# Optimization experiments

Hardware: AMD Instinct MI355X
Metric: run time of the kernel (lower is better)

The kernel has to match this reference:

```python
import jax, jax.numpy as jnp
import numpy as np
import itertools

B, DIM, RES = 128, 384, 16
NH, KD, D = 8, 32, 128            # heads, key_dim, d = attn_ratio*key_dim
NHKD, DH = NH * KD, NH * D        # 256, 1024
N = RES * RES                     # 256 tokens
SCALE = KD ** -0.5


def _bias_idxs():
    pts = list(itertools.product(range(RES), range(RES)))
    offsets, idxs = {}, []
    for p1 in pts:
        for p2 in pts:
            off = (abs(p1[0] - p2[0]), abs(p1[1] - p2[1]))
            if off not in offsets:
                offsets[off] = len(offsets)
            idxs.append(offsets[off])
    return np.array(idxs, dtype=np.int32).reshape(N, N), len(offsets)


def setup_inputs() -> dict:
    key = jax.random.key(0)
    ks = jax.random.split(key, 16)
    idxs, n_off = _bias_idxs()
    s = 0.02
    return {
        "x": jax.random.normal(ks[0], (B, DIM, RES, RES), jnp.float32),
        "q_w": jax.random.normal(ks[1], (NHKD, DIM), jnp.float32) * s,
        "q_b": jnp.zeros((NHKD,), jnp.float32),
        "k_w": jax.random.normal(ks[2], (NHKD, DIM), jnp.float32) * s,
        "k_b": jnp.zeros((NHKD,), jnp.float32),
        "v_w": jax.random.normal(ks[3], (DH, DIM), jnp.float32) * s,
        "v_b": jnp.zeros((DH,), jnp.float32),
        "vl_w": jax.random.normal(ks[4], (DH, 1, 3, 3), jnp.float32) * s,
        "vl_b": jnp.zeros((DH,), jnp.float32),
        "th1_w": jax.random.normal(ks[5], (NH, NH), jnp.float32) * s,
        "th1_b": jnp.zeros((NH,), jnp.float32),
        "th2_w": jax.random.normal(ks[6], (NH, NH), jnp.float32) * s,
        "th2_b": jnp.zeros((NH,), jnp.float32),
        "proj_w": jax.random.normal(ks[7], (DIM, DH), jnp.float32) * s,
        "proj_b": jnp.zeros((DIM,), jnp.float32),
        "attn_bias": jax.random.normal(ks[8], (NH, n_off), jnp.float32) * s,
        "bias_idxs": jnp.asarray(idxs),
    }


def _conv1x1(x, w, b):  # x: [B,C,H,W], w: [O,C]
    return jnp.einsum('bchw,oc->bohw', x, w) + b[:, None, None]


def reference(x, q_w, q_b, k_w, k_b, v_w, v_b, vl_w, vl_b,
              th1_w, th1_b, th2_w, th2_b, proj_w, proj_b,
              attn_bias, bias_idxs):
    Bx, C, H, W = x.shape
    q = _conv1x1(x, q_w, q_b).reshape(Bx, NH, KD, N).transpose(0, 1, 3, 2)  # bhnk
    k = _conv1x1(x, k_w, k_b).reshape(Bx, NH, KD, N)                        # bhkm
    v4 = _conv1x1(x, v_w, v_b)                                              # [B,DH,H,W]
    v_local = jax.lax.conv_general_dilated(
        v4, vl_w, window_strides=(1, 1), padding='SAME',
        dimension_numbers=('NCHW', 'OIHW', 'NCHW'),
        feature_group_count=DH) + vl_b[:, None, None]
    v = v4.reshape(Bx, NH, D, N).transpose(0, 1, 3, 2)                      # bhnd

    attn = jnp.einsum('bhnk,bhkm->bhnm', q, k) * SCALE + attn_bias[:, bias_idxs]
    attn = jnp.einsum('gh,bhnm->bgnm', th1_w, attn) + th1_b[:, None, None]  # talking head 1
    attn = jax.nn.softmax(attn, axis=-1)
    attn = jnp.einsum('gh,bhnm->bgnm', th2_w, attn) + th2_b[:, None, None]  # talking head 2

    o = jnp.einsum('bhnm,bhmd->bhnd', attn, v)
    out = o.transpose(0, 1, 3, 2).reshape(Bx, DH, H, W) + v_local
    out = jax.nn.relu(out)
    return _conv1x1(out, proj_w, proj_b)
```

## Files before the change

kernel.cpp:

```cpp
#include <hip/hip_runtime.h>
#include <hip/hip_bf16.h>

typedef __hip_bfloat16 bf16;
typedef __bf16 bf16v8 __attribute__((ext_vector_type(8)));
typedef float f32x4 __attribute__((ext_vector_type(4)));

#define BB    128
#define DIM   384
#define NTOK  256
#define NH    8
#define KD    32
#define DHEAD 128
#define DH    1024
#define SCALE 0.17677669529663687f
#define LOG2E 1.4426950408889634f

static __device__ __forceinline__ float sf(float x) {
  return (x == x) ? fminf(fmaxf(x, -1e4f), 1e4f) : 0.f;
}

static __device__ __forceinline__ float rfl(float x) {
  return __int_as_float(__builtin_amdgcn_readfirstlane(__float_as_int(x)));
}

#define GLOAD_LDS16(gsrc, ldst)                                                \
  __builtin_amdgcn_global_load_lds(                                            \
      (const __attribute__((address_space(1))) void*)(gsrc),                   \
      (__attribute__((address_space(3))) void*)(ldst), 16, 0, 0)

__global__ __launch_bounds__(256) void k_convert(const float* __restrict__ qw,
    const float* __restrict__ kw, const float* __restrict__ vw,
    const float* __restrict__ pw, bf16* __restrict__ dst) {
  int i = blockIdx.x * 256 + threadIdx.x;
  float v;
  if (i < 98304)       v = qw[i];
  else if (i < 196608) v = kw[i - 98304];
  else if (i < 589824) v = vw[i - 196608];
  else                 v = pw[i - 589824];
  dst[i] = __float2bfloat16(sf(v));
}

__global__ __launch_bounds__(256) void k_bias(const float* __restrict__ ab,
    const int* __restrict__ idxs, int n_off,
    const float* __restrict__ th1_w, const float* __restrict__ th1_b,
    float* __restrict__ bias_full) {
  int mn = blockIdx.x * 256 + threadIdx.x;
  int m = mn >> 8, n = mn & 255;
  int idx = idxs[n * 256 + m];
  float bh[8];
#pragma unroll
  for (int h = 0; h < 8; ++h) bh[h] = sf(ab[h * n_off + idx]);
#pragma unroll
  for (int g = 0; g < 8; ++g) {
    float a = sf(th1_b[g]);
#pragma unroll
    for (int h = 0; h < 8; ++h) a += sf(th1_w[g * 8 + h]) * bh[h];
    bias_full[((size_t)g * 256 + m) * 256 + n] = a * LOG2E;
  }
}

__global__ __launch_bounds__(256) void k_transpose_x(const float* __restrict__ x,
                                                     bf16* __restrict__ xT) {
  __shared__ bf16 tile[32][33];
  int b = blockIdx.z;
  int c0 = blockIdx.x * 32;
  int n0 = blockIdx.y * 32;
  int t = threadIdx.x;
  int tn = t & 31, tc = t >> 5;
#pragma unroll
  for (int p = 0; p < 4; ++p)
    tile[tc + p * 8][tn] =
        __float2bfloat16(sf(x[((size_t)b * DIM + c0 + tc + p * 8) * NTOK + n0 + tn]));
  __syncthreads();
  int wc = t & 31, wn = t >> 5;
#pragma unroll
  for (int p = 0; p < 4; ++p)
    xT[((size_t)b * NTOK + n0 + wn + p * 8) * DIM + c0 + wc] = tile[wc][wn + p * 8];
}

__global__ __launch_bounds__(256, 3) void k_qkv(const bf16* __restrict__ xT,
    const bf16* __restrict__ W, const float* __restrict__ q_b,
    const float* __restrict__ k_b, const float* __restrict__ v_b,
    bf16* __restrict__ qT, bf16* __restrict__ kT, bf16* __restrict__ v4,
    int nb) {
  __shared__ __align__(16) char smem[34816];
  bf16* sA = (bf16*)smem;
  bf16* sB = (bf16*)(smem + 16384);
  bf16* actt = (bf16*)smem;

  int id = blockIdx.x;
  int b, tile;
  if ((nb & 7) == 0) {
    int per = nb >> 3;
    int xcd = id & 7, slot = id >> 3;
    b = xcd * per + (slot % per);
    tile = slot / per;
  } else { b = id / 24; tile = id % 24; }
  int mt = tile >> 1, nt = tile & 1;
  int m0 = mt * 128, n0b = nt * 128;
  int t = threadIdx.x;
  int wave = t >> 6, lane = t & 63;
  int wm = wave >> 1, wn = wave & 1;
  int qd = lane >> 4, li = lane & 15;
  const bf16* xTb = xT + ((size_t)b * NTOK + n0b) * DIM;

  f32x4 acc[4][4];
#pragma unroll
  for (int r = 0; r < 4; ++r)
#pragma unroll
    for (int f = 0; f < 4; ++f) acc[r][f] = (f32x4){0.f, 0.f, 0.f, 0.f};

  for (int ks = 0; ks < 6; ++ks) {
    int k0 = ks * 64;
    __syncthreads();
#pragma unroll
    for (int i = 0; i < 8; ++i) {
      int g = wave * 512 + i * 64 + lane;
      int gg = g & 1023;
      int row = gg >> 3, slot = gg & 7;
      int col = ((slot ^ (row & 7)) << 3) + k0;
      const bf16* src = (g < 1024)
          ? (W + (size_t)(m0 + row) * DIM + col)
          : (xTb + (size_t)row * DIM + col);
      GLOAD_LDS16(src, smem + (size_t)(wave * 512 + i * 64) * 16);
    }
    __syncthreads();
#pragma unroll
    for (int s = 0; s < 2; ++s) {
      bf16v8 Afr[4], Bfr[4];
#pragma unroll
      for (int r = 0; r < 4; ++r) {
        int row = wm * 64 + r * 16 + li;
        Afr[r] = *(const bf16v8*)(sA + row * 64 + (((s * 4 + qd) ^ (row & 7)) << 3));
      }
#pragma unroll
      for (int f = 0; f < 4; ++f) {
        int row = wn * 64 + f * 16 + li;
        Bfr[f] = *(const bf16v8*)(sB + row * 64 + (((s * 4 + qd) ^ (row & 7)) << 3));
      }
#pragma unroll
      for (int r = 0; r < 4; ++r)
#pragma unroll
        for (int f = 0; f < 4; ++f)
          acc[r][f] = __builtin_amdgcn_mfma_f32_16x16x32_bf16(Afr[r], Bfr[f], acc[r][f], 0, 0, 0);
    }
  }
  __syncthreads();

  if (m0 >= 512) {
    int ch0 = m0 - 512;
#pragma unroll
    for (int r = 0; r < 4; ++r)
#pragma unroll
      for (int f = 0; f < 4; ++f) {
        int coll = wn * 64 + f * 16 + li;
#pragma unroll
        for (int rr = 0; rr < 4; ++rr) {
          int rowl = wm * 64 + r * 16 + qd * 4 + rr;
          actt[rowl * 136 + coll] =
              __float2bfloat16(acc[r][f][rr] + sf(v_b[ch0 + rowl]));
        }
      }
    __syncthreads();
#pragma unroll
    for (int it = 0; it < 8; ++it) {
      int g = it * 256 + t;
      int row = g >> 4, c16 = g & 15;
      bf16v8 vv = *(const bf16v8*)(actt + row * 136 + c16 * 8);
      *(bf16v8*)(v4 + ((size_t)b * DH + ch0 + row) * NTOK + n0b + c16 * 8) = vv;
    }
  } else {
    const float* bias = (m0 < 256) ? q_b : k_b;
    bf16* dst = (m0 < 256) ? qT : kT;
    int mb = (m0 < 256) ? m0 : m0 - 256;
#pragma unroll
    for (int r = 0; r < 4; ++r)
#pragma unroll
      for (int f = 0; f < 4; ++f) {
        int n = n0b + wn * 64 + f * 16 + li;
        int rowg = mb + wm * 64 + r * 16 + qd * 4;
        int h = rowg >> 5, kd = rowg & 31;
        union { bf16 e[4]; uint2 u; } pk;
#pragma unroll
        for (int rr = 0; rr < 4; ++rr)
          pk.e[rr] = __float2bfloat16(acc[r][f][rr] + sf(bias[rowg + rr]));
        *(uint2*)(dst + (((size_t)b * NH + h) * NTOK + n) * KD + kd) = pk.u;
      }
  }
}

__global__ __launch_bounds__(1024, 4) void k_scores(const bf16* __restrict__ qT,
    const bf16* __restrict__ kT, const float* __restrict__ bias_full,
    const float* __restrict__ th1_w,
    const float* __restrict__ th2_w, const float* __restrict__ th2_b,
    bf16* __restrict__ P, int nb) {
  __shared__ float s_th1[64], s_th2[64], s_t2b[8];
  __shared__ float s_part[16][8][16];
  __shared__ float s_invl[8][16];
  int t = threadIdx.x;
  if (t < 64) { s_th1[t] = sf(th1_w[t]) * (SCALE * LOG2E); s_th2[t] = sf(th2_w[t]); }
  if (t >= 64 && t < 72) s_t2b[t - 64] = sf(th2_b[t - 64]);
  int id = blockIdx.x;
  int b, nt;
  if ((nb & 7) == 0) {
    int per = nb >> 3;
    int xcd = id & 7, slot = id >> 3;
    b = xcd * per + (slot % per);
    nt = slot / per;
  } else { b = id >> 4; nt = id & 15; }
  int n0 = nt * 16;
  int wave = t >> 6, lane = t & 63, qd = lane >> 4, li = lane & 15;
  int ms = wave * 16;

  f32x4 S[8];
#pragma unroll
  for (int h = 0; h < 8; ++h) {
    bf16v8 Ak = *(const bf16v8*)(kT + (((size_t)b * NH + h) * NTOK + ms + li) * KD + qd * 8);
    bf16v8 Bq = *(const bf16v8*)(qT + (((size_t)b * NH + h) * NTOK + n0 + li) * KD + qd * 8);
    f32x4 c = {0.f, 0.f, 0.f, 0.f};
    S[h] = __builtin_amdgcn_mfma_f32_16x16x32_bf16(Ak, Bq, c, 0, 0, 0);
  }
  __syncthreads();

  f32x4 E[8];
  {
    float w1[64];
#pragma unroll
    for (int i = 0; i < 64; ++i) w1[i] = rfl(s_th1[i]);
#pragma unroll
    for (int r = 0; r < 4; ++r) {
#pragma unroll
      for (int g = 0; g < 8; ++g) {
        float a = bias_full[((size_t)g * 256 + ms + qd * 4 + r) * 256 + n0 + li];
#pragma unroll
        for (int h = 0; h < 8; ++h) a += w1[g * 8 + h] * S[h][r];
        E[g][r] = exp2f(fminf(a, 43.3f));
      }
    }
  }
#pragma unroll
  for (int g = 0; g < 8; ++g) {
    float v = (E[g][0] + E[g][1]) + (E[g][2] + E[g][3]);
    v += __shfl_xor(v, 16, 64);
    v += __shfl_xor(v, 32, 64);
    if (qd == 0) s_part[wave][g][li] = v;
  }
  __syncthreads();
  if (t < 128) {
    int g = t >> 4, n = t & 15;
    float ssum = 0.f;
#pragma unroll
    for (int w2 = 0; w2 < 16; ++w2) ssum += s_part[w2][g][n];
    s_invl[g][n] = 1.0f / ssum;
  }
  __syncthreads();
#pragma unroll
  for (int g = 0; g < 8; ++g) {
    float inv = s_invl[g][li];
#pragma unroll
    for (int r = 0; r < 4; ++r) E[g][r] *= inv;
  }

  {
    float w2[64], b2[8];
#pragma unroll
    for (int i = 0; i < 64; ++i) w2[i] = rfl(s_th2[i]);
#pragma unroll
    for (int i = 0; i < 8; ++i) b2[i] = rfl(s_t2b[i]);
    size_t pbase = (size_t)b * NH * 65536 + (size_t)nt * 4096 +
                   (size_t)(wave >> 1) * 512 + li * 32 + (wave & 1) * 16 + qd * 4;
#pragma unroll
    for (int g2 = 0; g2 < 8; ++g2) {
      union { bf16 e[4]; uint2 u; } pk;
#pragma unroll
      for (int r = 0; r < 4; ++r) {
        float a = b2[g2];
#pragma unroll
        for (int g = 0; g < 8; ++g) a += w2[g2 * 8 + g] * E[g][r];
        pk.e[r] = __float2bfloat16(a);
      }
      *(uint2*)(P + pbase + (size_t)g2 * 65536) = pk.u;
    }
  }
}

static __device__ __forceinline__ int vswz(int ch, int tok) {
  return tok ^ ((ch & 7) << 3);
}

__global__ __launch_bounds__(512, 4) void k_pv(const bf16* __restrict__ P,
    const bf16* __restrict__ v4,
    const float* __restrict__ vl_w, const float* __restrict__ vl_b,
    bf16* __restrict__ act, int nb) {
  __shared__ bf16 v_s[128][256];
  __shared__ float wv_s[1152];
  __shared__ float vb_s[128];
  __shared__ bf16 tbuf[8][16][20];
  int id = blockIdx.x;
  int b, h;
  if ((nb & 7) == 0) {
    int per = nb >> 3;
    int xcd = id & 7, slot = id >> 3;
    b = xcd * per + (slot % per);
    h = slot / per;
  } else { b = id >> 3; h = id & 7; }
  int t = threadIdx.x;
  int wave = t >> 6, lane = t & 63;
  int qd = lane >> 4, li = lane & 15;
  int nw = wave * 32;
  int nwt = wave * 2;
  const bf16* Pb = P + ((size_t)b * NH + h) * 65536;
  const bf16* Vb = v4 + ((size_t)b * DH + h * DHEAD) * NTOK;

  bf16v8 Af[4][2][2];
#pragma unroll
  for (int mi = 0; mi < 4; ++mi)
#pragma unroll
    for (int s = 0; s < 2; ++s)
#pragma unroll
      for (int r = 0; r < 2; ++r)
        Af[mi][s][r] = *(const bf16v8*)(Pb + (size_t)(nwt + r) * 4096 +
                                        (mi * 2 + s) * 512 + li * 32 + qd * 8);

#pragma unroll
  for (int p = 0; p < 8; ++p) {
    int idx = p * 512 + t;
    int ch = idx >> 5, tok = (idx & 31) * 8;
    *(bf16v8*)&v_s[ch][vswz(ch, tok)] = *(const bf16v8*)(Vb + (size_t)ch * NTOK + tok);
  }
  for (int i = t; i < 1152; i += 512) wv_s[i] = sf(vl_w[(size_t)h * DHEAD * 9 + i]);
  if (t < 128) vb_s[t] = sf(vl_b[h * DHEAD + t]);
  __syncthreads();

  f32x4 acc[2][8];
#pragma unroll
  for (int r = 0; r < 2; ++r)
#pragma unroll
    for (int f = 0; f < 8; ++f) acc[r][f] = (f32x4){0.f, 0.f, 0.f, 0.f};
#pragma unroll
  for (int mi = 0; mi < 4; ++mi) {
    int m0 = mi * 64;
#pragma unroll
    for (int s = 0; s < 2; ++s) {
      bf16v8 Bf[8];
#pragma unroll
      for (int f = 0; f < 8; ++f) {
        int ch = f * 16 + li;
        Bf[f] = *(const bf16v8*)&v_s[ch][vswz(ch, m0 + s * 32 + qd * 8)];
      }
#pragma unroll
      for (int f = 0; f < 8; ++f)
#pragma unroll
        for (int r = 0; r < 2; ++r)
          acc[r][f] = __builtin_amdgcn_mfma_f32_16x16x32_bf16(Af[mi][s][r], Bf[f], acc[r][f], 0, 0, 0);
    }
  }

#pragma unroll
  for (int f = 0; f < 8; ++f) {
    int chl = f * 16 + li;
    float wv[9];
#pragma unroll
    for (int j = 0; j < 9; ++j) wv[j] = wv_s[chl * 9 + j];
    float vb = vb_s[chl];
#pragma unroll
    for (int r = 0; r < 2; ++r) {
      int y = (nw + r * 16) >> 4;
      float vvv[3][6];
#pragma unroll
      for (int yy = 0; yy < 3; ++yy) {
        int y3 = y - 1 + yy;
        float e0 = 0.f, e1 = 0.f, e2 = 0.f, e3 = 0.f;
        if (y3 >= 0 && y3 < 16) {
          int tok = y3 * 16 + qd * 4;
          union { uint2 u; bf16 e[4]; } w4;
          w4.u = *(const uint2*)&v_s[chl][vswz(chl, tok)];
          e0 = __bfloat162float(w4.e[0]);
          e1 = __bfloat162float(w4.e[1]);
          e2 = __bfloat162float(w4.e[2]);
          e3 = __bfloat162float(w4.e[3]);
        }
        float lft = __shfl_up(e3, 16, 64);
        float rgt = __shfl_down(e0, 16, 64);
        if (qd == 0) lft = 0.f;
        if (qd == 3) rgt = 0.f;
        vvv[yy][0] = lft; vvv[yy][1] = e0; vvv[yy][2] = e1;
        vvv[yy][3] = e2;  vvv[yy][4] = e3; vvv[yy][5] = rgt;
      }
#pragma unroll
      for (int rr = 0; rr < 4; ++rr) {
        float s = vb;
#pragma unroll
        for (int yy = 0; yy < 3; ++yy)
#pragma unroll
          for (int j = 0; j < 3; ++j)
            s += vvv[yy][rr + j] * wv[yy * 3 + j];
        float v = fmaxf(acc[r][f][rr] + s, 0.f);
        tbuf[wave][qd * 4 + rr][li] = __float2bfloat16(v);
      }
      uint2 pr = *(const uint2*)&tbuf[wave][li][qd * 4];
      *(uint2*)(act + ((size_t)b * NTOK + nw + r * 16 + li) * DH +
                h * DHEAD + f * 16 + qd * 4) = pr;
    }
  }
}

__global__ __launch_bounds__(256, 4) void k_proj(const bf16* __restrict__ act,
    const bf16* __restrict__ proj_w, const float* __restrict__ proj_b,
    int b_base, int nb, float* __restrict__ out) {
  int id = blockIdx.x;
  int b, mt;
  if ((nb & 7) == 0) {
    int per = nb >> 3;
    int xcd = id & 7, slot = id >> 3;
    b = xcd * per + (slot % per);
    mt = slot / per;
  } else { b = id / 6; mt = id % 6; }
  int m0 = mt * 64;
  int bg = b_base + b;
  int wave = threadIdx.x >> 6, lane = threadIdx.x & 63;
  int qd = lane >> 4, li = lane & 15;
  int n0 = wave * 64;
  f32x4 acc[4][4];
#pragma unroll
  for (int r = 0; r < 4; ++r)
#pragma unroll
    for (int f = 0; f < 4; ++f) acc[r][f] = (f32x4){0.f, 0.f, 0.f, 0.f};
  for (int k0 = 0; k0 < DH; k0 += 32) {
    bf16v8 Af[4], Bf[4];
#pragma unroll
    for (int r = 0; r < 4; ++r)
      Af[r] = *(const bf16v8*)(proj_w + (size_t)(m0 + r * 16 + li) * DH + k0 + qd * 8);
#pragma unroll
    for (int f = 0; f < 4; ++f)
      Bf[f] = *(const bf16v8*)(act + ((size_t)b * NTOK + n0 + f * 16 + li) * DH + k0 + qd * 8);
#pragma unroll
    for (int r = 0; r < 4; ++r)
#pragma unroll
      for (int f = 0; f < 4; ++f)
        acc[r][f] = __builtin_amdgcn_mfma_f32_16x16x32_bf16(Af[r], Bf[f], acc[r][f], 0, 0, 0);
  }
#pragma unroll
  for (int r = 0; r < 4; ++r)
#pragma unroll
    for (int f = 0; f < 4; ++f) {
      int n = n0 + f * 16 + li;
#pragma unroll
      for (int rr = 0; rr < 4; ++rr) {
        int dim = m0 + r * 16 + qd * 4 + rr;
        out[((size_t)bg * DIM + dim) * NTOK + n] = acc[r][f][rr] + sf(proj_b[dim]);
      }
    }
}

extern "C" void kernel_launch(void* const* d_in, const int* in_sizes, int n_in,
                              void* d_out, int out_size, void* d_ws, size_t ws_size,
                              hipStream_t stream) {
  const float* x      = (const float*)d_in[0];
  const float* q_w    = (const float*)d_in[1];
  const float* q_b    = (const float*)d_in[2];
  const float* k_w    = (const float*)d_in[3];
  const float* k_b    = (const float*)d_in[4];
  const float* v_w    = (const float*)d_in[5];
  const float* v_b    = (const float*)d_in[6];
  const float* vl_w   = (const float*)d_in[7];
  const float* vl_b   = (const float*)d_in[8];
  const float* th1_w  = (const float*)d_in[9];
  const float* th1_b  = (const float*)d_in[10];
  const float* th2_w  = (const float*)d_in[11];
  const float* th2_b  = (const float*)d_in[12];
  const float* proj_w = (const float*)d_in[13];
  const float* proj_b = (const float*)d_in[14];
  const float* attn_b = (const float*)d_in[15];
  const int*   idxs   = (const int*)d_in[16];
  int n_off = in_sizes[15] / NH;
  float* out = (float*)d_out;

  const size_t WQ = 98304, WK = 98304, WV = 393216, WP = 393216;
  const size_t WTOT = WQ + WK + WV + WP;
  const size_t BFULL = (size_t)NH * NTOK * NTOK;
  const size_t PB_XT = (size_t)NTOK * DIM;
  const size_t PB_QK = (size_t)NH * NTOK * KD;
  const size_t PB_V  = (size_t)DH * NTOK;
  const size_t PB_AC = (size_t)NTOK * DH;
  const size_t PB_P  = (size_t)NH * NTOK * NTOK;
  const size_t perb  = (PB_XT + 2 * PB_QK + PB_V + PB_AC + PB_P) * 2;
  const size_t fixed = WTOT * 2 + BFULL * 4;

  char* w = (char*)d_ws;
  bf16* wcvt = (bf16*)w;  w += WTOT * 2;
  bf16* wq = wcvt;
  bf16* wk = wcvt + WQ;
  bf16* wv = wcvt + WQ + WK;
  bf16* wp = wcvt + WQ + WK + WV;
  float* bias_full = (float*)w;  w += BFULL * 4;

  size_t rem = (ws_size > fixed) ? (ws_size - fixed) : 0;
  int CH = (int)(rem / perb);
  if (CH > BB) CH = BB;
  if (CH >= 8) CH &= ~7;
  if (CH < 1) CH = 1;

  bf16* xT  = (bf16*)w;  w += (size_t)CH * PB_XT * 2;
  bf16* qT  = (bf16*)w;  w += (size_t)CH * PB_QK * 2;
  bf16* kT  = (bf16*)w;  w += (size_t)CH * PB_QK * 2;
  bf16* v4  = (bf16*)w;  w += (size_t)CH * PB_V * 2;
  bf16* act = (bf16*)w;  w += (size_t)CH * PB_AC * 2;
  bf16* P   = (bf16*)w;  w += (size_t)CH * PB_P * 2;

  k_convert<<<(int)(WTOT / 256), 256, 0, stream>>>(q_w, k_w, v_w, proj_w, wcvt);
  k_bias<<<256, 256, 0, stream>>>(attn_b, idxs, n_off, th1_w, th1_b, bias_full);

  for (int c0 = 0; c0 < BB; c0 += CH) {
    int cb = (BB - c0 < CH) ? (BB - c0) : CH;
    k_transpose_x<<<dim3(12, 8, cb), 256, 0, stream>>>(x + (size_t)c0 * DIM * NTOK, xT);
    k_qkv<<<cb * 24, 256, 0, stream>>>(xT, wcvt, q_b, k_b, v_b, qT, kT, v4, cb);
    k_scores<<<cb * 16, 1024, 0, stream>>>(qT, kT, bias_full,
                                           th1_w, th2_w, th2_b, P, cb);
    k_pv<<<cb * 16 / 2, 512, 0, stream>>>(P, v4, vl_w, vl_b, act, cb);
    k_proj<<<cb * 6, 256, 0, stream>>>(act, wp, proj_b, c0, cb, out);
  }
}
```

Before: 490.5 us.

## Stage proj GEMM tiles in LDS with swizzled layout and 128x128 block tiles

The output projection kernel now loads 128x64 slices of the weight and activation into shared memory using direct global-to-LDS loads with an XOR swizzle. Each block computes a 128x128 output tile with a 2x2 wave grid, where before each wave streamed its own fragments straight from global memory in a 64x256 tile. This is meant to cut redundant global/L2 traffic and improve reuse. The cost is two barriers per k-step with no double buffering, and occupancy drops from 4 to 3 blocks per CU.

```diff
diff --git a/kernel.cpp b/kernel.cpp
--- a/kernel.cpp
+++ b/kernel.cpp
@@ -405,49 +405,80 @@
   }
 }
 
-__global__ __launch_bounds__(256, 4) void k_proj(const bf16* __restrict__ act,
-    const bf16* __restrict__ proj_w, const float* __restrict__ proj_b,
+__global__ __launch_bounds__(256, 3) void k_proj(const bf16* __restrict__ act,
+    const bf16* __restrict__ Wp, const float* __restrict__ proj_b,
     int b_base, int nb, float* __restrict__ out) {
+  __shared__ __align__(16) char smem[32768];
+  bf16* sA = (bf16*)smem;
+  bf16* sB = (bf16*)(smem + 16384);
+
   int id = blockIdx.x;
-  int b, mt;
+  int b, tile;
   if ((nb & 7) == 0) {
     int per = nb >> 3;
     int xcd = id & 7, slot = id >> 3;
     b = xcd * per + (slot % per);
-    mt = slot / per;
-  } else { b = id / 6; mt = id % 6; }
-  int m0 = mt * 64;
+    tile = slot / per;
+  } else { b = id / 6; tile = id % 6; }
+  int mt = tile >> 1, nt = tile & 1;
+  int m0 = mt * 128, n0b = nt * 128;
   int bg = b_base + b;
-  int wave = threadIdx.x >> 6, lane = threadIdx.x & 63;
+  int t = threadIdx.x;
+  int wave = t >> 6, lane = t & 63;
+  int wm = wave >> 1, wn = wave & 1;
   int qd = lane >> 4, li = lane & 15;
-  int n0 = wave * 64;
+  const bf16* actb = act + ((size_t)b * NTOK + n0b) * DH;
+
   f32x4 acc[4][4];
 #pragma unroll
   for (int r = 0; r < 4; ++r)
 #pragma unroll
     for (int f = 0; f < 4; ++f) acc[r][f] = (f32x4){0.f, 0.f, 0.f, 0.f};
-  for (int k0 = 0; k0 < DH; k0 += 32) {
-    bf16v8 Af[4], Bf[4];
-#pragma unroll
-    for (int r = 0; r < 4; ++r)
-      Af[r] = *(const bf16v8*)(proj_w + (size_t)(m0 + r * 16 + li) * DH + k0 + qd * 8);
-#pragma unroll
-    for (int f = 0; f < 4; ++f)
-      Bf[f] = *(const bf16v8*)(act + ((size_t)b * NTOK + n0 + f * 16 + li) * DH + k0 + qd * 8);
-#pragma unroll
-    for (int r = 0; r < 4; ++r)
-#pragma unroll
-      for (int f = 0; f < 4; ++f)
-        acc[r][f] = __builtin_amdgcn_mfma_f32_16x16x32_bf16(Af[r], Bf[f], acc[r][f], 0, 0, 0);
-  }
+
+  for (int ks = 0; ks < 16; ++ks) {
+    int k0 = ks * 64;
+    __syncthreads();
+#pragma unroll
+    for (int i = 0; i < 8; ++i) {
+      int g = wave * 512 + i * 64 + lane;
+      int gg = g & 1023;
+      int row = gg >> 3, slot = gg & 7;
+      int col = ((slot ^ (row & 7)) << 3) + k0;
+      const bf16* src = (g < 1024)
+          ? (Wp + (size_t)(m0 + row) * DH + col)
+          : (actb + (size_t)row * DH + col);
+      GLOAD_LDS16(src, smem + (size_t)(wave * 512 + i * 64) * 16);
+    }
+    __syncthreads();
+#pragma unroll
+    for (int s = 0; s < 2; ++s) {
+      bf16v8 Afr[4], Bfr[4];
+#pragma unroll
+      for (int r = 0; r < 4; ++r) {
+        int row = wm * 64 + r * 16 + li;
+        Afr[r] = *(const bf16v8*)(sA + row * 64 + (((s * 4 + qd) ^ (row & 7)) << 3));
+      }
+#pragma unroll
+      for (int f = 0; f < 4; ++f) {
+        int row = wn * 64 + f * 16 + li;
+        Bfr[f] = *(const bf16v8*)(sB + row * 64 + (((s * 4 + qd) ^ (row & 7)) << 3));
+      }
+#pragma unroll
+      for (int r = 0; r < 4; ++r)
+#pragma unroll
+        for (int f = 0; f < 4; ++f)
+          acc[r][f] = __builtin_amdgcn_mfma_f32_16x16x32_bf16(Afr[r], Bfr[f], acc[r][f], 0, 0, 0);
+    }
+  }
+
 #pragma unroll
   for (int r = 0; r < 4; ++r)
 #pragma unroll
     for (int f = 0; f < 4; ++f) {
-      int n = n0 + f * 16 + li;
+      int n = n0b + wn * 64 + f * 16 + li;
 #pragma unroll
       for (int rr = 0; rr < 4; ++rr) {
-        int dim = m0 + r * 16 + qd * 4 + rr;
+        int dim = m0 + wm * 64 + r * 16 + qd * 4 + rr;
         out[((size_t)bg * DIM + dim) * NTOK + n] = acc[r][f][rr] + sf(proj_b[dim]);
       }
     }
```

Result: faster. 407.5 us (-16.9%).
